# Kernel tuning notes

Hardware: AMD Instinct MI355X
Metric: run time of the kernel (lower is better)

The kernel has to match this reference:

```python
import jax, jax.numpy as jnp
import numpy as np

# Config matching init_kwargs
N_SEGMENT = 8
N_GROUP = 8
K = 3            # correlation_neighbor
PAD = K // 2     # 1
BN_EPS = 1e-5


def setup_inputs() -> dict:
    key = jax.random.key(0)
    k1, k2, k3 = jax.random.split(key, 3)
    nt, c, h, w = 64, 256, 56, 56
    x = jax.random.normal(k1, (nt, c, h, w), dtype=jnp.float32)
    # Conv2d(72 -> 144, groups=8, kernel=1): weight [144, 9, 1, 1], bias [144]
    w_conv = jax.random.normal(k2, (144, 9, 1, 1), dtype=jnp.float32) * 0.1
    b_conv = jax.random.normal(k3, (144,), dtype=jnp.float32) * 0.1
    gamma = jnp.ones((c,), dtype=jnp.float32)
    beta = jnp.zeros((c,), dtype=jnp.float32)
    return {"x": x, "w_conv": w_conv, "b_conv": b_conv, "gamma": gamma, "beta": beta}


def reference(x, w_conv, b_conv, gamma, beta):
    nt, c, h, w = x.shape
    G = N_GROUP
    cg = c // G
    nt2 = nt // 2

    # ReplicationPad2d(1)
    xp = jnp.pad(x, ((0, 0), (0, 0), (PAD, PAD), (PAD, PAD)), mode="edge")
    x_even = x[::2]          # [nt2, c, h, w]
    xp_odd = xp[1::2]        # [nt2, c, h+2, w+2]

    # Cost volume: shifted multiply + per-group channel sum, 3x3 offsets
    corrs = []
    for i in range(K):
        for j in range(K):
            corr = x_even * jax.lax.slice(xp_odd, (0, 0, i, j), (nt2, c, i + h, j + w))
            corr = corr.reshape(nt2, G, cg, h, w).sum(axis=2)  # [nt2, G, h, w]
            corrs.append(corr)
    corr_feat = jnp.stack(corrs, axis=1)  # [nt2, 9, G, h, w] (offset outer, group inner)

    # Grouped 1x1 conv (groups=G): contiguous channel split of the [9*G] layout
    cr = corr_feat.reshape(nt2, G, K * K, h, w)               # [nt2, G, 9, h, w]
    wg = w_conv.reshape(G, 2 * K * K, K * K)                  # [G, 18, 9]
    xcorr = jnp.einsum("ngihw,goi->ngohw", cr, wg) + b_conv.reshape(1, G, 2 * K * K, 1, 1)
    # view(nt2, 3, 3, 2*G, h, w)
    xcorr = xcorr.reshape(nt2, K, K, 2 * G, h, w)

    # x_pad viewed as (nt, c_per_group, n_group, H+2, W+2)  (group is inner here!)
    xp2 = xp.reshape(nt, cg, G, h + 2, w + 2)
    xp_e = xp2[::2]   # even frames [nt2, cg, G, h+2, w+2]
    xp_o = xp2[1::2]  # odd frames

    # Weighted re-fusion over the 9 offsets (accumulate to avoid a big stack)
    acc = jnp.zeros((nt2, cg, G, h, w), dtype=x.dtype)
    for i in range(K):
        for j in range(K):
            we = xcorr[:, i, j, 0::2][:, None]  # [nt2, 1, G, h, w]
            wo = xcorr[:, i, j, 1::2][:, None]
            acc = acc + xp_e[:, :, :, i:i + h, j:j + w] * we \
                      + xp_o[:, :, :, i:i + h, j:j + w] * wo
    out = acc.reshape(nt2, c, h, w)  # (cg outer, G inner) flatten matches torch view

    # BatchNorm2d (training-mode batch statistics)
    mean = out.mean(axis=(0, 2, 3), keepdims=True)
    var = out.var(axis=(0, 2, 3), keepdims=True)
    out = (out - mean) * jax.lax.rsqrt(var + BN_EPS)
    out = out * gamma.reshape(1, c, 1, 1) + beta.reshape(1, c, 1, 1)
    return out
```

## Files before the change

### kernel.cpp

```cpp
#include <hip/hip_runtime.h>
#include <cstdint>

#define HW 3136
#define WID 56
#define NBLK 1792

__device__ __forceinline__ int clampi(int v, int lo, int hi) {
    return v < lo ? lo : (v > hi ? hi : v);
}

__device__ __forceinline__ float bperm(int a4, float v) {
    return __int_as_float(__builtin_amdgcn_ds_bpermute(a4, __float_as_int(v)));
}

__device__ __forceinline__ void fma2(float2& a, const float2& u, const float2& w) {
    a.x += u.x * w.x; a.y += u.y * w.y;
}

__global__ __launch_bounds__(256, 2) void tf_fused(
    const float* __restrict__ x, const float* __restrict__ wconv,
    const float* __restrict__ bconv, float* __restrict__ out)
{
    __shared__ float2 CP[2 * 9 * 28];
    __shared__ float  CR[72 * 56];

    const int d = blockIdx.x;
    const int logical = (d & 7) * 224 + (d >> 3);
    const int n  = logical / 56;
    const int r0 = logical % 56;
    const int t = threadIdx.x;
    const int wv = t >> 6;
    const int l = t & 63;
    const int sub = l >> 5;
    const int s8 = wv * 2 + sub;
    const int qd0 = l & 31;
    const bool act = qd0 < 28;
    const int qd = act ? qd0 : 27;

    const float* xe = x + (size_t)(2 * n) * 256 * HW;
    const float* xo = xe + (size_t)256 * HW;

    const int am = ((qd0 == 0) ? l : (l - 1)) * 4;
    const int ap = ((qd0 >= 27) ? l : (l + 1)) * 4;
    const bool le = (qd0 == 0);
    const bool re = (qd0 >= 27);

    int rb[3];
    #pragma unroll
    for (int di = 0; di < 3; ++di) rb[di] = clampi(r0 + di - 1, 0, 55) * WID + qd * 2;
    const int rc = r0 * WID + qd * 2;

#define MKTAPS2(v, Tm, Tp)                                  \
    {                                                       \
        const float lwp = bperm(am, (v).y);                 \
        const float rwp = bperm(ap, (v).x);                 \
        Tm = make_float2(le ? (v).x : lwp, (v).x);          \
        Tp = make_float2((v).y, re ? (v).y : rwp);          \
    }

    for (int g = 0; g < 8; ++g) {
        const int ch0 = g * 32 + 4 * s8;
        const float* pe = xe + (size_t)ch0 * HW;
        const float* po = xo + (size_t)ch0 * HW;

        float2 crg[9];
        #pragma unroll
        for (int i = 0; i < 9; ++i) crg[i] = make_float2(0.f, 0.f);

        #pragma unroll
        for (int c = 0; c < 4; ++c) {
            const float2 E = *(const float2*)(pe + (size_t)c * HW + rc);
            #pragma unroll
            for (int di = 0; di < 3; ++di) {
                const float2 O = *(const float2*)(po + (size_t)c * HW + rb[di]);
                float2 Tm, Tp;
                MKTAPS2(O, Tm, Tp)
                fma2(crg[di * 3 + 0], E, Tm);
                fma2(crg[di * 3 + 1], E, O);
                fma2(crg[di * 3 + 2], E, Tp);
            }
        }

        #pragma unroll
        for (int ij = 0; ij < 9; ++ij) {
            crg[ij].x += __shfl_xor(crg[ij].x, 32);
            crg[ij].y += __shfl_xor(crg[ij].y, 32);
        }

        if (wv < 2 && sub == 0 && act) {
            #pragma unroll
            for (int ij = 0; ij < 9; ++ij)
                CP[(wv * 9 + ij) * 28 + qd] = crg[ij];
        }
        __syncthreads();
        if (wv >= 2 && sub == 0 && act) {
            const int sl = wv - 2;
            #pragma unroll
            for (int ij = 0; ij < 9; ++ij) {
                float2 v = CP[(sl * 9 + ij) * 28 + qd];
                v.x += crg[ij].x; v.y += crg[ij].y;
                CP[(sl * 9 + ij) * 28 + qd] = v;
            }
        }
        __syncthreads();
        if (wv == 0 && sub == 0 && act) {
            #pragma unroll
            for (int ij = 0; ij < 9; ++ij) {
                const float2 v0 = CP[(0 * 9 + ij) * 28 + qd];
                const float2 v1 = CP[(1 * 9 + ij) * 28 + qd];
                float2 v;
                v.x = v0.x + v1.x;
                v.y = v0.y + v1.y;
                *(float2*)(CR + (ij * 8 + g) * 56 + qd * 2) = v;
            }
        }
        __syncthreads();
    }

    float2 We[9], Wo[9];
    #pragma unroll
    for (int ij = 0; ij < 9; ++ij) {
        const int fe = ij * 16 + 2 * s8;
        const int a = fe / 18;
        const float be = bconv[fe], bo = bconv[fe + 1];
        float2 we = make_float2(be, be);
        float2 wo = make_float2(bo, bo);
        #pragma unroll
        for (int b = 0; b < 9; ++b) {
            const float2 c2 = *(const float2*)(CR + (a * 9 + b) * 56 + qd * 2);
            const float wce = wconv[fe * 9 + b];
            const float wco = wconv[fe * 9 + 9 + b];
            we.x += c2.x * wce; we.y += c2.y * wce;
            wo.x += c2.x * wco; wo.y += c2.y * wco;
        }
        We[ij] = we; Wo[ij] = wo;
    }

    float* ob = out + (size_t)n * 256 * HW + r0 * WID + qd * 2;

    #pragma unroll 2
    for (int k = 0; k < 32; ++k) {
        const int ch = k * 8 + s8;
        const float* pe = xe + (size_t)ch * HW;
        const float* po = xo + (size_t)ch * HW;

        float2 acc = make_float2(0.f, 0.f);
        #pragma unroll
        for (int di = 0; di < 3; ++di) {
            const float2 Ev = *(const float2*)(pe + rb[di]);
            const float2 Ov = *(const float2*)(po + rb[di]);
            float2 TEm, TEp, TOm, TOp;
            MKTAPS2(Ev, TEm, TEp)
            MKTAPS2(Ov, TOm, TOp)
            fma2(acc, TEm, We[di * 3 + 0]); fma2(acc, TOm, Wo[di * 3 + 0]);
            fma2(acc, Ev,  We[di * 3 + 1]); fma2(acc, Ov,  Wo[di * 3 + 1]);
            fma2(acc, TEp, We[di * 3 + 2]); fma2(acc, TOp, Wo[di * 3 + 2]);
        }
        if (act) *(float2*)(ob + (size_t)ch * HW) = acc;
    }
#undef MKTAPS2
}

__global__ void tf_stats_part(const float* __restrict__ out,
                              float* __restrict__ ps, float* __restrict__ pq)
{
    const int ch = blockIdx.x >> 3;
    const int sl = blockIdx.x & 7;
    const int t = threadIdx.x;

    float s = 0.f, q = 0.f;
    #pragma unroll
    for (int k = 0; k < 4; ++k) {
        const float4* p = (const float4*)(out + ((size_t)(4 * sl + k) * 256 + ch) * HW);
        for (int i = t; i < 784; i += 256) {
            const float4 v = p[i];
            s += v.x + v.y + v.z + v.w;
            q += v.x * v.x + v.y * v.y + v.z * v.z + v.w * v.w;
        }
    }
    #pragma unroll
    for (int o = 32; o >= 1; o >>= 1) {
        s += __shfl_xor(s, o);
        q += __shfl_xor(q, o);
    }
    __shared__ float rs[4], rq[4];
    if ((t & 63) == 0) { rs[t >> 6] = s; rq[t >> 6] = q; }
    __syncthreads();
    if (t == 0) {
        ps[blockIdx.x] = rs[0] + rs[1] + rs[2] + rs[3];
        pq[blockIdx.x] = rq[0] + rq[1] + rq[2] + rq[3];
    }
}

__global__ void tf_stats_fin(const float* __restrict__ ps, const float* __restrict__ pq,
                             const float* __restrict__ gamma, const float* __restrict__ beta,
                             float* __restrict__ AB)
{
    const int ch = threadIdx.x;
    float s = 0.f, q = 0.f;
    #pragma unroll
    for (int sl = 0; sl < 8; ++sl) {
        s += ps[ch * 8 + sl];
        q += pq[ch * 8 + sl];
    }
    const float inv = 1.f / 100352.f;
    const float mean = s * inv;
    const float var = q * inv - mean * mean;
    const float rstd = rsqrtf(var + 1e-5f);
    const float A = gamma[ch] * rstd;
    AB[ch] = A;
    AB[256 + ch] = beta[ch] - mean * A;
}

__global__ void tf_norm(float* __restrict__ out, const float* __restrict__ AB)
{
    const unsigned total4 = 32u * 256u * 784u;
    unsigned i = blockIdx.x * 256u + threadIdx.x;
    const unsigned stride = gridDim.x * 256u;
    float4* o4 = (float4*)out;
    for (; i < total4; i += stride) {
        const unsigned ch = (i / 784u) & 255u;
        const float A = AB[ch], B = AB[256 + ch];
        float4 v = o4[i];
        v.x = v.x * A + B;
        v.y = v.y * A + B;
        v.z = v.z * A + B;
        v.w = v.w * A + B;
        o4[i] = v;
    }
}

extern "C" void kernel_launch(void* const* d_in, const int* in_sizes, int n_in,
                              void* d_out, int out_size, void* d_ws, size_t ws_size,
                              hipStream_t stream) {
    const float* x     = (const float*)d_in[0];
    const float* wconv = (const float*)d_in[1];
    const float* bconv = (const float*)d_in[2];
    const float* gamma = (const float*)d_in[3];
    const float* beta  = (const float*)d_in[4];
    float* out = (float*)d_out;

    float* ps = (float*)d_ws;
    float* pq = ps + 2048;
    float* AB = pq + 2048;

    tf_fused<<<NBLK, 256, 0, stream>>>(x, wconv, bconv, out);
    tf_stats_part<<<2048, 256, 0, stream>>>(out, ps, pq);
    tf_stats_fin<<<1, 256, 0, stream>>>(ps, pq, gamma, beta, AB);
    tf_norm<<<2048, 256, 0, stream>>>(out, AB);
}
```

Measured before the change: 192.7 us.

## Pack even/odd frames into interleaved bf16 pairs before fused correlation kernel

Adds a pre-pass that converts the fp32 input to bf16 and interleaves each even frame with its odd partner in one 32-bit word. The fused correlation and re-fusion kernel then reads one word per pixel per channel to get both frames, with one pixel per lane, which halves the traffic of its repeated input reads. In exchange it pays for a full extra read of x and a write of the packed buffer, and it lowers input precision to bf16, which may push the result past the accuracy tolerance. The old fp32 path is kept as a fallback when the workspace is too small.

```diff
diff --git a/kernel.cpp b/kernel.cpp
--- a/kernel.cpp
+++ b/kernel.cpp
@@ -5,19 +5,163 @@
 #define WID 56
 #define NBLK 1792
 
+typedef float f4v __attribute__((ext_vector_type(4)));
+
 __device__ __forceinline__ int clampi(int v, int lo, int hi) {
     return v < lo ? lo : (v > hi ? hi : v);
 }
-
+__device__ __forceinline__ uint32_t rne16(float f) {
+    uint32_t b = __float_as_uint(f);
+    return (b + 0x7fffu + ((b >> 16) & 1u)) >> 16;
+}
+__device__ __forceinline__ float blo(uint32_t u) { return __uint_as_float(u << 16); }
+__device__ __forceinline__ float bhi(uint32_t u) { return __uint_as_float(u & 0xffff0000u); }
+__device__ __forceinline__ uint32_t bpermu(int a4, uint32_t v) {
+    return (uint32_t)__builtin_amdgcn_ds_bpermute(a4, (int)v);
+}
 __device__ __forceinline__ float bperm(int a4, float v) {
     return __int_as_float(__builtin_amdgcn_ds_bpermute(a4, __float_as_int(v)));
 }
-
 __device__ __forceinline__ void fma2(float2& a, const float2& u, const float2& w) {
     a.x += u.x * w.x; a.y += u.y * w.y;
 }
 
-__global__ __launch_bounds__(256, 2) void tf_fused(
+__global__ __launch_bounds__(256) void tf_pack(const float* __restrict__ x,
+                                               uint32_t* __restrict__ xb)
+{
+    const unsigned total4 = 8192u * 784u;
+    unsigned i = blockIdx.x * 256u + threadIdx.x;
+    const unsigned stride = gridDim.x * 256u;
+    for (; i < total4; i += stride) {
+        const unsigned p4 = i / 784u;
+        const unsigned i4 = i - p4 * 784u;
+        const unsigned pair = p4 >> 8;
+        const size_t eoff = ((size_t)pair * 512 + (p4 & 255u)) * HW + i4 * 4;
+        const f4v e = __builtin_nontemporal_load((const f4v*)(x + eoff));
+        const f4v o = __builtin_nontemporal_load((const f4v*)(x + eoff + (size_t)256 * HW));
+        uint4 u;
+        u.x = (rne16(o.x) << 16) | rne16(e.x);
+        u.y = (rne16(o.y) << 16) | rne16(e.y);
+        u.z = (rne16(o.z) << 16) | rne16(e.z);
+        u.w = (rne16(o.w) << 16) | rne16(e.w);
+        *(uint4*)(xb + (size_t)p4 * HW + i4 * 4) = u;
+    }
+}
+
+__global__ __launch_bounds__(256, 2) void tf_fused_bf(
+    const uint32_t* __restrict__ xb, const float* __restrict__ wconv,
+    const float* __restrict__ bconv, float* __restrict__ out)
+{
+    __shared__ float CP[2 * 9 * 56];
+    __shared__ float CR[72 * 56];
+
+    const int d = blockIdx.x;
+    const int logical = (d & 7) * 224 + (d >> 3);
+    const int n  = logical / 56;
+    const int r0 = logical % 56;
+    const int t = threadIdx.x;
+    const int su = __builtin_amdgcn_readfirstlane(t >> 6);
+    const int lane = t & 63;
+    const bool act = lane < WID;
+    const int px = act ? lane : 55;
+
+    const uint32_t* xq = xb + (size_t)n * 256 * HW;
+
+    const int am = clampi(lane - 1, 0, 55) * 4;
+    const int ap = clampi(lane + 1, 0, 55) * 4;
+
+    const int rb0 = clampi(r0 - 1, 0, 55) * WID + px;
+    const int rb1 = r0 * WID + px;
+    const int rb2 = clampi(r0 + 1, 0, 55) * WID + px;
+
+    for (int g = 0; g < 8; ++g) {
+        float crg[9];
+        #pragma unroll
+        for (int i = 0; i < 9; ++i) crg[i] = 0.f;
+
+        #pragma unroll
+        for (int sub = 0; sub < 4; ++sub) {
+            const int ch0 = (g * 4 + sub) * 8 + 2 * su;
+            #pragma unroll
+            for (int c = 0; c < 2; ++c) {
+                const uint32_t* base = xq + (size_t)(ch0 + c) * HW;
+                const uint32_t u0 = base[rb0], u1 = base[rb1], u2 = base[rb2];
+                const float e = blo(u1);
+                {   const uint32_t um = bpermu(am, u0), up = bpermu(ap, u0);
+                    crg[0] += e * bhi(um); crg[1] += e * bhi(u0); crg[2] += e * bhi(up); }
+                {   const uint32_t um = bpermu(am, u1), up = bpermu(ap, u1);
+                    crg[3] += e * bhi(um); crg[4] += e * bhi(u1); crg[5] += e * bhi(up); }
+                {   const uint32_t um = bpermu(am, u2), up = bpermu(ap, u2);
+                    crg[6] += e * bhi(um); crg[7] += e * bhi(u2); crg[8] += e * bhi(up); }
+            }
+        }
+        if (su < 2 && act) {
+            #pragma unroll
+            for (int ij = 0; ij < 9; ++ij) CP[(su * 9 + ij) * 56 + px] = crg[ij];
+        }
+        __syncthreads();
+        if (su >= 2 && act) {
+            const int sl = su - 2;
+            #pragma unroll
+            for (int ij = 0; ij < 9; ++ij) CP[(sl * 9 + ij) * 56 + px] += crg[ij];
+        }
+        __syncthreads();
+        if (su == 0 && act) {
+            #pragma unroll
+            for (int ij = 0; ij < 9; ++ij)
+                CR[(ij * 8 + g) * 56 + px] =
+                    CP[(0 * 9 + ij) * 56 + px] + CP[(1 * 9 + ij) * 56 + px];
+        }
+        __syncthreads();
+    }
+
+    float Wv[9][4];
+    #pragma unroll
+    for (int ij = 0; ij < 9; ++ij)
+        #pragma unroll
+        for (int j = 0; j < 4; ++j) {
+            const int f = ij * 16 + 4 * su + j;
+            const int a = f / 18;
+            float w = bconv[f];
+            #pragma unroll
+            for (int b = 0; b < 9; ++b)
+                w += CR[(a * 9 + b) * 56 + px] * wconv[f * 9 + b];
+            Wv[ij][j] = w;
+        }
+
+    float* ob = out + (size_t)n * 256 * HW + r0 * WID;
+
+    #pragma unroll 2
+    for (int q = 0; q < 32; ++q) {
+        const int ch0 = q * 8 + 2 * su;
+        float a0 = 0.f, a1 = 0.f;
+        #pragma unroll
+        for (int c = 0; c < 2; ++c) {
+            const uint32_t* base = xq + (size_t)(ch0 + c) * HW;
+            const uint32_t u0 = base[rb0], u1 = base[rb1], u2 = base[rb2];
+            float acc = 0.f;
+            {   const uint32_t um = bpermu(am, u0), up = bpermu(ap, u0);
+                acc += blo(um) * Wv[0][2 * c] + bhi(um) * Wv[0][2 * c + 1];
+                acc += blo(u0) * Wv[1][2 * c] + bhi(u0) * Wv[1][2 * c + 1];
+                acc += blo(up) * Wv[2][2 * c] + bhi(up) * Wv[2][2 * c + 1]; }
+            {   const uint32_t um = bpermu(am, u1), up = bpermu(ap, u1);
+                acc += blo(um) * Wv[3][2 * c] + bhi(um) * Wv[3][2 * c + 1];
+                acc += blo(u1) * Wv[4][2 * c] + bhi(u1) * Wv[4][2 * c + 1];
+                acc += blo(up) * Wv[5][2 * c] + bhi(up) * Wv[5][2 * c + 1]; }
+            {   const uint32_t um = bpermu(am, u2), up = bpermu(ap, u2);
+                acc += blo(um) * Wv[6][2 * c] + bhi(um) * Wv[6][2 * c + 1];
+                acc += blo(u2) * Wv[7][2 * c] + bhi(u2) * Wv[7][2 * c + 1];
+                acc += blo(up) * Wv[8][2 * c] + bhi(up) * Wv[8][2 * c + 1]; }
+            if (c == 0) a0 = acc; else a1 = acc;
+        }
+        if (act) {
+            ob[(size_t)ch0 * HW + px] = a0;
+            ob[(size_t)(ch0 + 1) * HW + px] = a1;
+        }
+    }
+}
+
+__global__ __launch_bounds__(256, 2) void tf_fused_f32(
     const float* __restrict__ x, const float* __restrict__ wconv,
     const float* __restrict__ bconv, float* __restrict__ out)
 {
@@ -62,11 +206,9 @@
         const int ch0 = g * 32 + 4 * s8;
         const float* pe = xe + (size_t)ch0 * HW;
         const float* po = xo + (size_t)ch0 * HW;
-
         float2 crg[9];
         #pragma unroll
         for (int i = 0; i < 9; ++i) crg[i] = make_float2(0.f, 0.f);
-
         #pragma unroll
         for (int c = 0; c < 4; ++c) {
             const float2 E = *(const float2*)(pe + (size_t)c * HW + rc);
@@ -80,17 +222,14 @@
                 fma2(crg[di * 3 + 2], E, Tp);
             }
         }
-
         #pragma unroll
         for (int ij = 0; ij < 9; ++ij) {
             crg[ij].x += __shfl_xor(crg[ij].x, 32);
             crg[ij].y += __shfl_xor(crg[ij].y, 32);
         }
-
         if (wv < 2 && sub == 0 && act) {
             #pragma unroll
-            for (int ij = 0; ij < 9; ++ij)
-                CP[(wv * 9 + ij) * 28 + qd] = crg[ij];
+            for (int ij = 0; ij < 9; ++ij) CP[(wv * 9 + ij) * 28 + qd] = crg[ij];
         }
         __syncthreads();
         if (wv >= 2 && sub == 0 && act) {
@@ -109,8 +248,7 @@
                 const float2 v0 = CP[(0 * 9 + ij) * 28 + qd];
                 const float2 v1 = CP[(1 * 9 + ij) * 28 + qd];
                 float2 v;
-                v.x = v0.x + v1.x;
-                v.y = v0.y + v1.y;
+                v.x = v0.x + v1.x; v.y = v0.y + v1.y;
                 *(float2*)(CR + (ij * 8 + g) * 56 + qd * 2) = v;
             }
         }
@@ -137,13 +275,11 @@
     }
 
     float* ob = out + (size_t)n * 256 * HW + r0 * WID + qd * 2;
-
     #pragma unroll 2
     for (int k = 0; k < 32; ++k) {
         const int ch = k * 8 + s8;
         const float* pe = xe + (size_t)ch * HW;
         const float* po = xo + (size_t)ch * HW;
-
         float2 acc = make_float2(0.f, 0.f);
         #pragma unroll
         for (int di = 0; di < 3; ++di) {
@@ -243,8 +379,15 @@
     float* ps = (float*)d_ws;
     float* pq = ps + 2048;
     float* AB = pq + 2048;
-
-    tf_fused<<<NBLK, 256, 0, stream>>>(x, wconv, bconv, out);
+    uint32_t* xbuf = (uint32_t*)((uint8_t*)d_ws + 32768);
+    const size_t need = 32768 + (size_t)32 * 256 * HW * 4;
+
+    if (ws_size >= need) {
+        tf_pack<<<4096, 256, 0, stream>>>(x, xbuf);
+        tf_fused_bf<<<NBLK, 256, 0, stream>>>(xbuf, wconv, bconv, out);
+    } else {
+        tf_fused_f32<<<NBLK, 256, 0, stream>>>(x, wconv, bconv, out);
+    }
     tf_stats_part<<<2048, 256, 0, stream>>>(out, ps, pq);
     tf_stats_fin<<<1, 256, 0, stream>>>(ps, pq, gamma, beta, AB);
     tf_norm<<<2048, 256, 0, stream>>>(out, AB);
```

New measurement: 203.9 us. +5.8%, slower.
